# Kernel tuning notes

Measured on AMD Instinct MI355X. Metric: run time of the kernel, lower is better.

Reference implementation:

```python
import jax, jax.numpy as jnp
import numpy as np

B, N, D, O, K, E = 16, 10000, 128, 64, 3, 160000


def setup_inputs() -> dict:
    key = jax.random.key(0)
    k1, k2, k3, k4, k5 = jax.random.split(key, 5)
    x = jax.random.normal(k1, (B, N, D), dtype=jnp.float32)
    W = jax.random.normal(k2, (K, D, O), dtype=jnp.float32) * (1.0 / np.sqrt(D))
    sup_vals = jax.random.uniform(k3, (K, E), dtype=jnp.float32)
    sup_row = jax.random.randint(k4, (K, E), 0, N, dtype=jnp.int32)
    sup_col = jax.random.randint(k5, (K, E), 0, N, dtype=jnp.int32)
    return {"x": x, "W": W, "sup_vals": sup_vals, "sup_row": sup_row, "sup_col": sup_col}


def reference(x, W, sup_vals, sup_row, sup_col):
    # x: [B, N, D]; W: [K, D, O]; supports as COO edge lists per support.
    # dropout=0.0 (keep_prob=1) -> identity; act=None -> identity; agg='concat'.
    num_nodes = x.shape[1]
    num_supports = W.shape[0]
    outs = []
    for i in range(num_supports):
        # dense feature transform, laid out node-major for the SpMM: [N, B, O]
        pre = jnp.einsum('bnd,do->nbo', x, W[i])
        # SpMM: out[r] += A[r,c] * pre[c]  via gather + segment_sum
        gathered = pre[sup_col[i]] * sup_vals[i][:, None, None]  # [E, B, O]
        agg = jax.ops.segment_sum(gathered, sup_row[i], num_segments=num_nodes)  # [N, B, O]
        outs.append(jnp.transpose(agg, (1, 0, 2)))  # [B, N, O]
    return jnp.concatenate(outs, axis=-1)  # [B, N, O*K]
```

## Files before the change

### kernel.cpp

```cpp
#include <hip/hip_runtime.h>
#include <hip/hip_bf16.h>

constexpr int B = 16, N = 10000, D = 128, O = 64, K = 3, E = 160000;
constexpr int BO = B * O;
constexpr int KO = K * O;
constexpr int NPB = 8;

using short8  = __attribute__((ext_vector_type(8))) short;
using floatx4 = __attribute__((ext_vector_type(4))) float;
struct U4 { unsigned a, b, c, d; };

__device__ __forceinline__ float bf2f(unsigned short u) {
  return __uint_as_float(((unsigned int)u) << 16);
}
__device__ __forceinline__ unsigned short f2bf(float f) {
  return (unsigned short)((__float_as_uint(f) + 0x8000u) >> 16);
}
__device__ __forceinline__ unsigned pkbf(float lo, float hi) {
  return ((__float_as_uint(lo) + 0x8000u) >> 16) |
         ((__float_as_uint(hi) + 0x8000u) & 0xFFFF0000u);
}

__global__ void wpack_kernel(const float* __restrict__ w, unsigned short* __restrict__ wp) {
  const int i = blockIdx.x * 64 + threadIdx.x;
  if (i >= K * 16 * 64) return;
  const int lane = i & 63;
  const int dd = (i >> 6) & 3;
  const int t4 = (i >> 8) & 3;
  const int k  = i >> 10;
  const int o  = t4 * 16 + (lane & 15);
  const int d0 = dd * 32 + (lane >> 4) * 8;
  unsigned short* dst = wp + (size_t)i * 8;
#pragma unroll
  for (int j = 0; j < 8; ++j)
    dst[j] = f2bf(w[((size_t)k * D + d0 + j) * O + o]);
}

__global__ __launch_bounds__(192) void gemm_mfma_kernel(
    const float* __restrict__ x, const unsigned short* __restrict__ wpk,
    unsigned short* __restrict__ pre, int kBase)
{
  const int t = threadIdx.x;
  const int kloc = t >> 6;
  const int k = kBase + kloc;
  const int lane = t & 63;
  const int col  = lane & 15;
  const int quad = lane >> 4;

  short8 wfr[4][4];
#pragma unroll
  for (int t4 = 0; t4 < 4; ++t4)
#pragma unroll
    for (int dd = 0; dd < 4; ++dd)
      wfr[t4][dd] = *(const short8*)(wpk + (size_t)(((k * 4 + t4) * 4 + dd) * 64 + lane) * 8);

  const int n0 = blockIdx.x * NPB;
  const float* xbase = x + (size_t)col * N * D;

  for (int nn = 0; nn < NPB; ++nn) {
    const int n = n0 + nn;
    const float* xp = xbase + (size_t)n * D + quad * 8;
    short8 xfr[4];
#pragma unroll
    for (int dd = 0; dd < 4; ++dd) {
      const float4 lo = *(const float4*)(xp + dd * 32);
      const float4 hi = *(const float4*)(xp + dd * 32 + 4);
      U4 u;
      u.a = pkbf(lo.x, lo.y); u.b = pkbf(lo.z, lo.w);
      u.c = pkbf(hi.x, hi.y); u.d = pkbf(hi.z, hi.w);
      xfr[dd] = __builtin_bit_cast(short8, u);
    }

    floatx4 acc[4] = {};
#pragma unroll
    for (int dd = 0; dd < 4; ++dd)
#pragma unroll
      for (int t4 = 0; t4 < 4; ++t4)
        acc[t4] = __builtin_amdgcn_mfma_f32_16x16x32_bf16(wfr[t4][dd], xfr[dd], acc[t4], 0, 0, 0);

    unsigned short* pp = pre + (((size_t)kloc * N + n) << 10) + col * 64 + quad * 4;
#pragma unroll
    for (int t4 = 0; t4 < 4; ++t4) {
      uint2 pk2;
      pk2.x = pkbf(acc[t4][0], acc[t4][1]);
      pk2.y = pkbf(acc[t4][2], acc[t4][3]);
      *(uint2*)(pp + t4 * 16) = pk2;
    }
  }
}

__global__ void hist_kernel(const int* __restrict__ row, int* __restrict__ cnt) {
  const int i = blockIdx.x * 256 + threadIdx.x;
  if (i >= K * E) return;
  const int k = i / E;
  atomicAdd(&cnt[k * N + row[i]], 1);
}

__global__ __launch_bounds__(1024) void scan_kernel(int* __restrict__ cnt,
                                                    int* __restrict__ offs) {
  const int k = blockIdx.x;
  const int t = threadIdx.x;
  const int lane = t & 63, wid = t >> 6;
  __shared__ int wt[16];
  __shared__ int sbase;
  if (t == 0) { sbase = 0; offs[k * (N + 1)] = 0; }
  __syncthreads();

  for (int c0 = 0; c0 < N; c0 += 1024) {
    const int i = c0 + t;
    const int v = (i < N) ? cnt[k * N + i] : 0;
    int incl = v;
#pragma unroll
    for (int st = 1; st < 64; st <<= 1) {
      const int u = __shfl_up(incl, st, 64);
      if (lane >= st) incl += u;
    }
    if (lane == 63) wt[wid] = incl;
    __syncthreads();
    if (wid == 0) {
      int wv = (lane < 16) ? wt[lane] : 0;
#pragma unroll
      for (int st = 1; st < 16; st <<= 1) {
        const int u = __shfl_up(wv, st, 64);
        if (lane >= st) wv += u;
      }
      if (lane < 16) wt[lane] = wv;
    }
    __syncthreads();
    const int base = sbase + ((wid > 0) ? wt[wid - 1] : 0);
    if (i < N) {
      offs[k * (N + 1) + i + 1] = base + incl;
      cnt[k * N + i] = base + incl - v;
    }
    __syncthreads();
    if (t == 0) sbase += wt[15];
    __syncthreads();
  }
}

__global__ void scatter_kernel(const int* __restrict__ row, const int* __restrict__ col,
                               const float* __restrict__ vals,
                               int* __restrict__ cursor, int* __restrict__ scol,
                               float* __restrict__ sval) {
  const int i = blockIdx.x * 256 + threadIdx.x;
  if (i >= K * E) return;
  const int k = i / E;
  const int pos = atomicAdd(&cursor[k * N + row[i]], 1);
  scol[k * E + pos] = col[i];
  sval[k * E + pos] = vals[i];
}

__global__ __launch_bounds__(128) void spmm_kernel(
    const unsigned short* __restrict__ pre, const int* __restrict__ offs,
    const int* __restrict__ scol, const float* __restrict__ sval,
    float* __restrict__ out, int kBase)
{
  const int bid = blockIdx.x;
  const int kloc = bid / N;
  const int n = bid - kloc * N;
  const int k = kBase + kloc;
  const int t = threadIdx.x;
  const int j0 = __builtin_amdgcn_readfirstlane(offs[k * (N + 1) + n]);
  const int j1 = __builtin_amdgcn_readfirstlane(offs[k * (N + 1) + n + 1]);
  const unsigned short* pk = pre + (((size_t)kloc * N) << 10) + 8 * t;
  const int* cj = scol + (size_t)k * E;
  const float* vj = sval + (size_t)k * E;

  float a[8] = {};
  int j = j0;
  for (; j + 3 < j1; j += 4) {
    const int c0 = __builtin_amdgcn_readfirstlane(cj[j]);
    const int c1 = __builtin_amdgcn_readfirstlane(cj[j + 1]);
    const int c2 = __builtin_amdgcn_readfirstlane(cj[j + 2]);
    const int c3 = __builtin_amdgcn_readfirstlane(cj[j + 3]);
    const float v0 = vj[j], v1 = vj[j + 1], v2 = vj[j + 2], v3 = vj[j + 3];
    const short8 u0 = *(const short8*)(pk + ((size_t)c0 << 10));
    const short8 u1 = *(const short8*)(pk + ((size_t)c1 << 10));
    const short8 u2 = *(const short8*)(pk + ((size_t)c2 << 10));
    const short8 u3 = *(const short8*)(pk + ((size_t)c3 << 10));
#pragma unroll
    for (int q = 0; q < 8; ++q)
      a[q] += v0 * bf2f((unsigned short)u0[q]) + v1 * bf2f((unsigned short)u1[q]) +
              v2 * bf2f((unsigned short)u2[q]) + v3 * bf2f((unsigned short)u3[q]);
  }
  for (; j < j1; ++j) {
    const int c0 = __builtin_amdgcn_readfirstlane(cj[j]);
    const float v0 = vj[j];
    const short8 u0 = *(const short8*)(pk + ((size_t)c0 << 10));
#pragma unroll
    for (int q = 0; q < 8; ++q)
      a[q] += v0 * bf2f((unsigned short)u0[q]);
  }

  const int b = t >> 3;
  const int o0 = (t & 7) * 8;
  float* op = out + ((size_t)b * N + n) * KO + (size_t)k * O + o0;
  *(float4*)op = *(const float4*)&a[0];
  *(float4*)(op + 4) = *(const float4*)&a[4];
}

extern "C" void kernel_launch(void* const* d_in, const int* in_sizes, int n_in,
                              void* d_out, int out_size, void* d_ws, size_t ws_size,
                              hipStream_t stream) {
  const float* x    = (const float*)d_in[0];
  const float* w    = (const float*)d_in[1];
  const float* vals = (const float*)d_in[2];
  const int* row    = (const int*)d_in[3];
  const int* col    = (const int*)d_in[4];
  float* out        = (float*)d_out;

  char* p = (char*)d_ws;
  int* offs = (int*)p;            p += ((size_t)K * (N + 1) * 4 + 15) & ~(size_t)15;
  int* cnt  = (int*)p;            p += (size_t)K * N * 4;
  int* scol = (int*)p;            p += (size_t)K * E * 4;
  float* sval = (float*)p;        p += (size_t)K * E * 4;
  unsigned short* wpk = (unsigned short*)p; p += (size_t)K * 16 * 64 * 8 * 2;
  unsigned short* pre = (unsigned short*)p;
  const size_t fixed = (size_t)(p - (char*)d_ws);
  const size_t preFull = (size_t)K * N * BO * 2;
  const bool full = ws_size >= fixed + preFull;

  hipMemsetAsync(cnt, 0, (size_t)K * N * 4, stream);

  wpack_kernel<<<48, 64, 0, stream>>>(w, wpk);
  const int eb = (K * E + 255) / 256;
  hist_kernel<<<eb, 256, 0, stream>>>(row, cnt);
  scan_kernel<<<K, 1024, 0, stream>>>(cnt, offs);
  scatter_kernel<<<eb, 256, 0, stream>>>(row, col, vals, cnt, scol, sval);

  if (full) {
    gemm_mfma_kernel<<<N / NPB, 64 * K, 0, stream>>>(x, wpk, pre, 0);
    spmm_kernel<<<K * N, 128, 0, stream>>>(pre, offs, scol, sval, out, 0);
  } else {
    for (int k = 0; k < K; ++k) {
      gemm_mfma_kernel<<<N / NPB, 64, 0, stream>>>(x, wpk, pre, k);
      spmm_kernel<<<N, 128, 0, stream>>>(pre, offs, scol, sval, out, k);
    }
  }
  (void)in_sizes; (void)n_in; (void)out_size;
}
```

Before: 419.9 us.

## Split SpMM feature columns across wavefront groups and process row chunks per block

The SpMM is restructured so that each 64-thread block handles one 128-column slice of the B*O feature vector for 8 consecutive rows. Previously one 128-thread block handled a full row. Each lane now gathers 4 bytes per edge instead of 16, and the edge loop is unrolled by 8 to keep more loads in flight. Neighbouring blocks with the same row chunk but different slices should reuse the column index and value reads through cache. The cost is narrower per-lane loads and index/value lists that are read once per slice, which adds per-edge scalar overhead.

New measurement: 397.3 us. 1.06x faster.

```diff
diff --git a/kernel.cpp b/kernel.cpp
--- a/kernel.cpp
+++ b/kernel.cpp
@@ -5,6 +5,9 @@
 constexpr int BO = B * O;
 constexpr int KO = K * O;
 constexpr int NPB = 8;
+constexpr int G = 8;
+constexpr int ROWS = 8;
+constexpr int NCH = N / ROWS;
 
 using short8  = __attribute__((ext_vector_type(8))) short;
 using floatx4 = __attribute__((ext_vector_type(4))) float;
@@ -150,53 +153,57 @@
   sval[k * E + pos] = vals[i];
 }
 
-__global__ __launch_bounds__(128) void spmm_kernel(
+__global__ __launch_bounds__(64) void spmm_kernel(
     const unsigned short* __restrict__ pre, const int* __restrict__ offs,
     const int* __restrict__ scol, const float* __restrict__ sval,
     float* __restrict__ out, int kBase)
 {
   const int bid = blockIdx.x;
-  const int kloc = bid / N;
-  const int n = bid - kloc * N;
+  const int g   = bid & 7;
+  const int t2  = bid >> 3;
+  const int nc  = t2 % NCH;
+  const int kloc = t2 / NCH;
   const int k = kBase + kloc;
-  const int t = threadIdx.x;
-  const int j0 = __builtin_amdgcn_readfirstlane(offs[k * (N + 1) + n]);
-  const int j1 = __builtin_amdgcn_readfirstlane(offs[k * (N + 1) + n + 1]);
-  const unsigned short* pk = pre + (((size_t)kloc * N) << 10) + 8 * t;
+  const int lane = threadIdx.x;
+
+  const int bo = g * 128 + 2 * lane;
+  const int b = bo >> 6;
+  const int o = bo & 63;
+  const unsigned short* pk = pre + (((size_t)kloc * N) << 10) + bo;
   const int* cj = scol + (size_t)k * E;
   const float* vj = sval + (size_t)k * E;
-
-  float a[8] = {};
-  int j = j0;
-  for (; j + 3 < j1; j += 4) {
-    const int c0 = __builtin_amdgcn_readfirstlane(cj[j]);
-    const int c1 = __builtin_amdgcn_readfirstlane(cj[j + 1]);
-    const int c2 = __builtin_amdgcn_readfirstlane(cj[j + 2]);
-    const int c3 = __builtin_amdgcn_readfirstlane(cj[j + 3]);
-    const float v0 = vj[j], v1 = vj[j + 1], v2 = vj[j + 2], v3 = vj[j + 3];
-    const short8 u0 = *(const short8*)(pk + ((size_t)c0 << 10));
-    const short8 u1 = *(const short8*)(pk + ((size_t)c1 << 10));
-    const short8 u2 = *(const short8*)(pk + ((size_t)c2 << 10));
-    const short8 u3 = *(const short8*)(pk + ((size_t)c3 << 10));
-#pragma unroll
-    for (int q = 0; q < 8; ++q)
-      a[q] += v0 * bf2f((unsigned short)u0[q]) + v1 * bf2f((unsigned short)u1[q]) +
-              v2 * bf2f((unsigned short)u2[q]) + v3 * bf2f((unsigned short)u3[q]);
-  }
-  for (; j < j1; ++j) {
-    const int c0 = __builtin_amdgcn_readfirstlane(cj[j]);
-    const float v0 = vj[j];
-    const short8 u0 = *(const short8*)(pk + ((size_t)c0 << 10));
-#pragma unroll
-    for (int q = 0; q < 8; ++q)
-      a[q] += v0 * bf2f((unsigned short)u0[q]);
-  }
-
-  const int b = t >> 3;
-  const int o0 = (t & 7) * 8;
-  float* op = out + ((size_t)b * N + n) * KO + (size_t)k * O + o0;
-  *(float4*)op = *(const float4*)&a[0];
-  *(float4*)(op + 4) = *(const float4*)&a[4];
+  const int* op = offs + k * (N + 1) + nc * ROWS;
+
+  for (int r = 0; r < ROWS; ++r) {
+    const int j0 = __builtin_amdgcn_readfirstlane(op[r]);
+    const int j1 = __builtin_amdgcn_readfirstlane(op[r + 1]);
+    float a0 = 0.f, a1 = 0.f;
+    int j = j0;
+    for (; j + 7 < j1; j += 8) {
+      unsigned u[8]; float v[8];
+#pragma unroll
+      for (int i = 0; i < 8; ++i) {
+        const int c = __builtin_amdgcn_readfirstlane(cj[j + i]);
+        u[i] = *(const unsigned*)(pk + ((size_t)c << 10));
+        v[i] = vj[j + i];
+      }
+#pragma unroll
+      for (int i = 0; i < 8; ++i) {
+        a0 += v[i] * bf2f((unsigned short)(u[i] & 0xFFFFu));
+        a1 += v[i] * bf2f((unsigned short)(u[i] >> 16));
+      }
+    }
+    for (; j < j1; ++j) {
+      const int c = __builtin_amdgcn_readfirstlane(cj[j]);
+      const float v = vj[j];
+      const unsigned u = *(const unsigned*)(pk + ((size_t)c << 10));
+      a0 += v * bf2f((unsigned short)(u & 0xFFFFu));
+      a1 += v * bf2f((unsigned short)(u >> 16));
+    }
+    const int n = nc * ROWS + r;
+    float2 st; st.x = a0; st.y = a1;
+    *(float2*)(out + ((size_t)b * N + n) * KO + (size_t)k * O + o) = st;
+  }
 }
 
 extern "C" void kernel_launch(void* const* d_in, const int* in_sizes, int n_in,
@@ -230,11 +237,11 @@
 
   if (full) {
     gemm_mfma_kernel<<<N / NPB, 64 * K, 0, stream>>>(x, wpk, pre, 0);
-    spmm_kernel<<<K * N, 128, 0, stream>>>(pre, offs, scol, sval, out, 0);
+    spmm_kernel<<<K * NCH * G, 64, 0, stream>>>(pre, offs, scol, sval, out, 0);
   } else {
     for (int k = 0; k < K; ++k) {
       gemm_mfma_kernel<<<N / NPB, 64, 0, stream>>>(x, wpk, pre, k);
-      spmm_kernel<<<N, 128, 0, stream>>>(pre, offs, scol, sval, out, k);
+      spmm_kernel<<<NCH * G, 64, 0, stream>>>(pre, offs, scol, sval, out, k);
     }
   }
   (void)in_sizes; (void)n_in; (void)out_size;
```
